# Kernel optimization log

Measured on AMD Instinct MI355X. Metric: run time of the kernel, lower is better.

Reference implementation:

```python
import jax, jax.numpy as jnp
import numpy as np

N_HEAD = 16

def setup_inputs() -> dict:
    key = jax.random.key(0)
    k1, k2 = jax.random.split(key)
    B, T, C = 4, 2048, 1024
    x = jax.random.normal(k1, (B, T, C), dtype=jnp.float32)
    # fused QKV projection weight, stored as [C, 3C] so qkv = x @ w_qkv
    # (equivalent to torch Linear(C, 3C, bias=False) with weight.T)
    w_qkv = jax.random.normal(k2, (C, 3 * C), dtype=jnp.float32) * (1.0 / np.sqrt(C))
    return {"x": x, "w_qkv": w_qkv}

def reference(x, w_qkv):
    B, T, C = x.shape
    H = N_HEAD
    D = C // H
    qkv = x @ w_qkv                                  # [B, T, 3C]
    q, k, v = jnp.split(qkv, 3, axis=2)              # each [B, T, C]
    q = q.reshape(B, T, H, D).transpose(0, 2, 1, 3)  # [B, H, T, D]
    k = k.reshape(B, T, H, D).transpose(0, 2, 1, 3)
    v = v.reshape(B, T, H, D).transpose(0, 2, 1, 3)
    scale = np.float32(1.0 / np.sqrt(D))
    att = jnp.einsum('bhqd,bhkd->bhqk', q, k) * scale   # [B, H, T, T]
    causal = jnp.tril(jnp.ones((T, T), dtype=bool))     # lower-tri = visible
    att = jnp.where(causal, att, -jnp.inf)
    att = jax.nn.softmax(att, axis=-1)
    out = jnp.einsum('bhqk,bhkd->bhqd', att, v)          # [B, H, T, D]
    return out.transpose(0, 2, 1, 3).reshape(B, T, C)
```

## Files before the change

### kernel.cpp

```cpp
#include <hip/hip_runtime.h>


#define B_ 4
#define T_ 2048
#define C_ 1024
#define H_ 16
#define D_ 64
#define QKV1 (B_*H_*T_*D_)

typedef __attribute__((ext_vector_type(4))) float  f32x4;
typedef __attribute__((ext_vector_type(8))) short  bf16x8;
typedef __attribute__((ext_vector_type(4))) short  bf16x4;

__device__ inline unsigned short f2bf(float f) {
  unsigned int u = __builtin_bit_cast(unsigned int, f);
  u += 0x7FFFu + ((u >> 16) & 1u);
  return (unsigned short)(u >> 16);
}

__device__ inline void gload16(const unsigned short* g, unsigned short* l) {
  __builtin_amdgcn_global_load_lds(
      (const __attribute__((address_space(1))) void*)g,
      (__attribute__((address_space(3))) void*)l, 16, 0, 0);
}

__global__ __launch_bounds__(256) void prep(const float* __restrict__ x,
                                            unsigned short* __restrict__ xb,
                                            const float* __restrict__ w,
                                            unsigned short* __restrict__ wt) {
  if (blockIdx.x < 2048) {
    size_t i = ((size_t)blockIdx.x * 256 + threadIdx.x) * 16;
    f32x4 a = *(const f32x4*)(x + i);
    f32x4 b = *(const f32x4*)(x + i + 4);
    f32x4 c = *(const f32x4*)(x + i + 8);
    f32x4 d = *(const f32x4*)(x + i + 12);
    bf16x8 o0, o1;
#pragma unroll
    for (int j = 0; j < 4; j++) {
      o0[j]     = (short)f2bf(a[j]);
      o0[j + 4] = (short)f2bf(b[j]);
      o1[j]     = (short)f2bf(c[j]);
      o1[j + 4] = (short)f2bf(d[j]);
    }
    *(bf16x8*)(xb + i) = o0;
    *(bf16x8*)(xb + i + 8) = o1;
  } else {
    __shared__ float tile[32][33];
    const int bid = blockIdx.x - 2048;
    const int tx = threadIdx.x & 31, ty = threadIdx.x >> 5;
    const int n0 = (bid % 96) * 32, k0 = (bid / 96) * 32;
#pragma unroll
    for (int j = 0; j < 4; j++) {
      int k = ty + j * 8;
      tile[k][tx] = w[(size_t)(k0 + k) * 3072 + n0 + tx];
    }
    __syncthreads();
#pragma unroll
    for (int j = 0; j < 4; j++) {
      int n = ty + j * 8;
      wt[(size_t)(n0 + n) * 1024 + k0 + tx] = f2bf(tile[tx][n]);
    }
  }
}

__global__ __launch_bounds__(256) void qkv_gemm(const unsigned short* __restrict__ xb,
                                                const unsigned short* __restrict__ wt,
                                                unsigned short* __restrict__ qkv) {
  __shared__ unsigned short Al[128 * 64];
  __shared__ unsigned short Bl[128 * 64];
  const int tid = threadIdx.x;
  const int lane = tid & 63, wid = tid >> 6;
  const int l15 = lane & 15, g = lane >> 4;
  const int m0 = blockIdx.y * 128, n0 = blockIdx.x * 128;
  const int wm = (wid >> 1) * 64, wn = (wid & 1) * 64;

  f32x4 acc[4][4] = {};

  const int srow[4] = { (0 * 256 + tid) >> 3, (1 * 256 + tid) >> 3,
                        (2 * 256 + tid) >> 3, (3 * 256 + tid) >> 3 };
  int scol[4];
#pragma unroll
  for (int sw = 0; sw < 4; sw++) {
    int s = sw * 256 + tid;
    scol[sw] = (s & 7) ^ (srow[sw] & 7);
  }

  for (int k0 = 0; k0 < 1024; k0 += 64) {
    __syncthreads();
#pragma unroll
    for (int sw = 0; sw < 4; sw++) {
      unsigned short* ldsA = &Al[(sw * 256 + wid * 64) * 8];
      unsigned short* ldsB = &Bl[(sw * 256 + wid * 64) * 8];
      gload16(xb + (size_t)(m0 + srow[sw]) * 1024 + k0 + scol[sw] * 8, ldsA);
      gload16(wt + (size_t)(n0 + srow[sw]) * 1024 + k0 + scol[sw] * 8, ldsB);
    }
    __syncthreads();

#pragma unroll
    for (int ks = 0; ks < 2; ks++) {
      bf16x8 af[4], bfr[4];
#pragma unroll
      for (int mt = 0; mt < 4; mt++) {
        int row = wm + mt * 16 + l15;
        int c = (ks * 4 + g) ^ (row & 7);
        af[mt] = *(const bf16x8*)&Al[(row * 8 + c) * 8];
      }
#pragma unroll
      for (int nt = 0; nt < 4; nt++) {
        int row = wn + nt * 16 + l15;
        int c = (ks * 4 + g) ^ (row & 7);
        bfr[nt] = *(const bf16x8*)&Bl[(row * 8 + c) * 8];
      }
#pragma unroll
      for (int mt = 0; mt < 4; mt++)
#pragma unroll
        for (int nt = 0; nt < 4; nt++)
          acc[mt][nt] = __builtin_amdgcn_mfma_f32_16x16x32_bf16(af[mt], bfr[nt], acc[mt][nt], 0, 0, 0);
    }
  }

  const int r0 = g * 4, cc = l15;
#pragma unroll
  for (int mt = 0; mt < 4; mt++)
#pragma unroll
    for (int nt = 0; nt < 4; nt++)
#pragma unroll
      for (int r = 0; r < 4; r++) {
        int m = m0 + wm + mt * 16 + r0 + r;
        int n = n0 + wn + nt * 16 + cc;
        int b = m >> 11, t = m & 2047;
        int which = n >> 10, c = n & 1023;
        int h = c >> 6, d = c & 63;
        qkv[(size_t)which * QKV1 + ((size_t)((b * H_ + h) * T_ + t)) * D_ + d] =
            f2bf(acc[mt][nt][r]);
      }
}

__global__ __launch_bounds__(256, 2) void attn(const unsigned short* __restrict__ qkv,
                                               float* __restrict__ out) {
  __shared__ unsigned short Kl[64][72];
  __shared__ unsigned short Vl[64][72];
  __shared__ unsigned short Pl[4][16][72];
  __shared__ float RSb[4][16], RSa[4][16];
  const int tid = threadIdx.x, lane = tid & 63, wq = tid >> 6;
  const int l15 = lane & 15, g = lane >> 4;
  const int bh = blockIdx.y;
  const int tt = bh >> 4;
  const int uu = ((int)blockIdx.x + (tt >> 1)) & 15;
  const int px = (tt & 1) ? (15 - uu) : uu;
  const int qta = px, qtb = 31 - px;
  const int ntiles = qtb + 1;
  const size_t base = (size_t)bh * (T_ * D_);
  const unsigned short* qp = qkv + base;
  const unsigned short* kp = qkv + (size_t)QKV1 + base;
  const unsigned short* vp = qkv + 2 * (size_t)QKV1 + base;

  bf16x8 qfa[2], qfb[2];
#define LOADQ(QF, Q0)                                                          \
  do {                                                                         \
    int qrow_ = (Q0) + wq * 16 + l15;                                          \
    _Pragma("unroll")                                                          \
    for (int kc = 0; kc < 2; kc++) {                                           \
      bf16x8 v = *(const bf16x8*)(qp + (size_t)qrow_ * 64 + kc * 32 + g * 8);  \
      _Pragma("unroll")                                                        \
      for (int j = 0; j < 8; j++) {                                            \
        unsigned short u = (unsigned short)v[j];                               \
        int e = u & 0x7F80;                                                    \
        u = (e > (3 << 7)) ? (unsigned short)(u - (3 << 7))                    \
                           : (unsigned short)(u & 0x8000);                     \
        v[j] = (short)u;                                                       \
      }                                                                        \
      QF[kc] = v;                                                              \
    }                                                                          \
  } while (0)
  LOADQ(qfa, qta * 64);
  LOADQ(qfb, qtb * 64);

  f32x4 oa[4] = {}, ob[4] = {};
  float rsa = 0.f, rsb = 0.f;

  bf16x8 kreg0, kreg1, vreg0, vreg1;
  const int krow = tid >> 3, kch = tid & 7;
  const int vpr = tid >> 3, vdch = tid & 7;
#define LOADKV(IT)                                                             \
  do {                                                                         \
    size_t k0_ = (size_t)(IT) * 64;                                            \
    kreg0 = *(const bf16x8*)(kp + (k0_ + krow) * 64 + kch * 8);                \
    kreg1 = *(const bf16x8*)(kp + (k0_ + 32 + krow) * 64 + kch * 8);           \
    vreg0 = *(const bf16x8*)(vp + (k0_ + 2 * vpr) * 64 + vdch * 8);            \
    vreg1 = *(const bf16x8*)(vp + (k0_ + 2 * vpr + 1) * 64 + vdch * 8);        \
  } while (0)

#define SOFTMAXT(S, RS, Q0, ISDIAG, K0)                                        \
  do {                                                                         \
    if (ISDIAG) {                                                              \
      _Pragma("unroll")                                                        \
      for (int nt = 0; nt < 4; nt++) {                                         \
        _Pragma("unroll")                                                      \
        for (int r = 0; r < 4; r++) {                                          \
          int kg_ = (K0) + nt * 16 + g * 4 + r;                                \
          if (kg_ > (Q0) + wq * 16 + l15) S[nt][r] = -1e30f;                   \
        }                                                                      \
      }                                                                        \
    }                                                                          \
    _Pragma("unroll")                                                          \
    for (int nt = 0; nt < 4; nt++) {                                           \
      bf16x4 pw_;                                                              \
      _Pragma("unroll")                                                        \
      for (int r = 0; r < 4; r++) {                                            \
        float p_ = __expf(S[nt][r]);                                           \
        RS += p_;                                                              \
        pw_[r] = (short)f2bf(p_);                                              \
      }                                                                        \
      *(bf16x4*)&Pl[wq][l15][nt * 16 + g * 4] = pw_;                           \
    }                                                                          \
  } while (0)

  LOADKV(0);
  for (int it = 0; it < ntiles; ++it) {
    __syncthreads();
    *(bf16x8*)&Kl[krow][kch * 8] = kreg0;
    *(bf16x8*)&Kl[32 + krow][kch * 8] = kreg1;
#pragma unroll
    for (int j = 0; j < 8; j++) {
      int d = vdch * 8 + j;
      unsigned int pk = ((unsigned int)(unsigned short)vreg1[j] << 16) |
                        (unsigned int)(unsigned short)vreg0[j];
      *(unsigned int*)&Vl[d][(2 * vpr) ^ ((d >> 3) << 3)] = pk;
    }
    if (it + 1 < ntiles) LOADKV(it + 1);
    __syncthreads();

    const bool doA = (it <= qta);

    f32x4 sb[4], sa[4];
    __builtin_amdgcn_s_setprio(1);
#pragma unroll
    for (int nt = 0; nt < 4; nt++) {
      bf16x8 kf0 = *(const bf16x8*)&Kl[nt * 16 + l15][g * 8];
      bf16x8 kf1 = *(const bf16x8*)&Kl[nt * 16 + l15][32 + g * 8];
      f32x4 t0 = {0.f, 0.f, 0.f, 0.f};
      t0 = __builtin_amdgcn_mfma_f32_16x16x32_bf16(kf0, qfb[0], t0, 0, 0, 0);
      t0 = __builtin_amdgcn_mfma_f32_16x16x32_bf16(kf1, qfb[1], t0, 0, 0, 0);
      sb[nt] = t0;
      if (doA) {
        f32x4 t1 = {0.f, 0.f, 0.f, 0.f};
        t1 = __builtin_amdgcn_mfma_f32_16x16x32_bf16(kf0, qfa[0], t1, 0, 0, 0);
        t1 = __builtin_amdgcn_mfma_f32_16x16x32_bf16(kf1, qfa[1], t1, 0, 0, 0);
        sa[nt] = t1;
      }
    }
    __builtin_amdgcn_s_setprio(0);

    SOFTMAXT(sb, rsb, qtb * 64, it == qtb, it * 64);
    asm volatile("s_waitcnt lgkmcnt(0)" ::: "memory");
    bf16x8 pb0 = *(const bf16x8*)&Pl[wq][l15][g * 8];
    bf16x8 pb1 = *(const bf16x8*)&Pl[wq][l15][32 + g * 8];

    bf16x8 pa0, pa1;
    if (doA) {
      SOFTMAXT(sa, rsa, qta * 64, it == qta, it * 64);
      asm volatile("s_waitcnt lgkmcnt(0)" ::: "memory");
      pa0 = *(const bf16x8*)&Pl[wq][l15][g * 8];
      pa1 = *(const bf16x8*)&Pl[wq][l15][32 + g * 8];
    }

    __builtin_amdgcn_s_setprio(1);
#pragma unroll
    for (int dt = 0; dt < 4; dt++) {
      int d_ = dt * 16 + l15;
      int sw_ = (d_ >> 3) << 3;
      bf16x8 vf0 = *(const bf16x8*)&Vl[d_][(g * 8) ^ sw_];
      bf16x8 vf1 = *(const bf16x8*)&Vl[d_][(32 + g * 8) ^ sw_];
      ob[dt] = __builtin_amdgcn_mfma_f32_16x16x32_bf16(pb0, vf0, ob[dt], 0, 0, 0);
      ob[dt] = __builtin_amdgcn_mfma_f32_16x16x32_bf16(pb1, vf1, ob[dt], 0, 0, 0);
      if (doA) {
        oa[dt] = __builtin_amdgcn_mfma_f32_16x16x32_bf16(pa0, vf0, oa[dt], 0, 0, 0);
        oa[dt] = __builtin_amdgcn_mfma_f32_16x16x32_bf16(pa1, vf1, oa[dt], 0, 0, 0);
      }
    }
    __builtin_amdgcn_s_setprio(0);
  }

  {
    float tb = rsb;
    tb += __shfl_xor(tb, 16); tb += __shfl_xor(tb, 32);
    float ta = rsa;
    ta += __shfl_xor(ta, 16); ta += __shfl_xor(ta, 32);
    if (g == 0) {
      RSb[wq][l15] = 1.0f / tb;
      RSa[wq][l15] = 1.0f / ta;
    }
  }
  asm volatile("s_waitcnt lgkmcnt(0)" ::: "memory");
  const int b = bh >> 4, h = bh & 15;
#define EPILOG(OACC, RSL, Q0)                                                  \
  do {                                                                         \
    _Pragma("unroll")                                                          \
    for (int r = 0; r < 4; r++) {                                              \
      float inv_ = RSL[wq][g * 4 + r];                                         \
      int qg_ = (Q0) + wq * 16 + g * 4 + r;                                    \
      _Pragma("unroll")                                                        \
      for (int dt = 0; dt < 4; dt++)                                           \
        out[((size_t)(b * T_ + qg_)) * C_ + h * 64 + dt * 16 + l15] =          \
            OACC[dt][r] * inv_;                                                \
    }                                                                          \
  } while (0)
  EPILOG(ob, RSb, qtb * 64);
  EPILOG(oa, RSa, qta * 64);
}

extern "C" void kernel_launch(void* const* d_in, const int* in_sizes, int n_in,
                              void* d_out, int out_size, void* d_ws, size_t ws_size,
                              hipStream_t stream) {
  const float* x = (const float*)d_in[0];
  const float* w = (const float*)d_in[1];
  float* out = (float*)d_out;
  unsigned short* wt  = (unsigned short*)d_ws;
  unsigned short* qkv = wt + (size_t)3072 * 1024;
  unsigned short* xb  = (unsigned short*)d_out;

  prep       <<<5120, 256, 0, stream>>>(x, xb, w, wt);
  qkv_gemm   <<<dim3(24, 64), 256, 0, stream>>>(xb, wt, qkv);
  attn       <<<dim3(16, 64), 256, 0, stream>>>(qkv, out);
}
```

Measured before the change: 145.2 us.

## Triple-buffer QKV GEMM with 256x128 tiles and 8 waves, interleaving prefetch with MFMA

Rewrites the QKV projection GEMM to use 512-thread blocks with 256x128 output tiles and a 3-stage LDS ring filled by async global-to-LDS loads. Each iteration issues the next-next tile's loads in slices between MFMA groups and uses a vmcnt wait plus a single barrier, instead of two barriers with no overlap. It also raises wave priority around the MFMAs. The aim is to hide global load latency and cut synchronisation in the GEMM. In exchange it uses more LDS (about 144KB) per block, which lowers occupancy, and adds hand-tuned waitcnt logic.

```diff
diff --git a/kernel.cpp b/kernel.cpp
--- a/kernel.cpp
+++ b/kernel.cpp
@@ -63,76 +63,112 @@
   }
 }
 
-__global__ __launch_bounds__(256) void qkv_gemm(const unsigned short* __restrict__ xb,
+__global__ __launch_bounds__(512) void qkv_gemm(const unsigned short* __restrict__ xb,
                                                 const unsigned short* __restrict__ wt,
                                                 unsigned short* __restrict__ qkv) {
-  __shared__ unsigned short Al[128 * 64];
-  __shared__ unsigned short Bl[128 * 64];
+  __shared__ unsigned short Al[3][256 * 64];
+  __shared__ unsigned short Bl[3][128 * 64];
   const int tid = threadIdx.x;
   const int lane = tid & 63, wid = tid >> 6;
   const int l15 = lane & 15, g = lane >> 4;
-  const int m0 = blockIdx.y * 128, n0 = blockIdx.x * 128;
-  const int wm = (wid >> 1) * 64, wn = (wid & 1) * 64;
-
-  f32x4 acc[4][4] = {};
-
-  const int srow[4] = { (0 * 256 + tid) >> 3, (1 * 256 + tid) >> 3,
-                        (2 * 256 + tid) >> 3, (3 * 256 + tid) >> 3 };
-  int scol[4];
+  const int m0 = blockIdx.y * 256, n0 = blockIdx.x * 128;
+  const int wr = wid >> 2, wc = wid & 3;
+
+  f32x4 acc[8][2] = {};
+
+  int arow[4], acol[4], brow[2], bcol[2];
 #pragma unroll
   for (int sw = 0; sw < 4; sw++) {
-    int s = sw * 256 + tid;
-    scol[sw] = (s & 7) ^ (srow[sw] & 7);
-  }
-
-  for (int k0 = 0; k0 < 1024; k0 += 64) {
-    __syncthreads();
-#pragma unroll
-    for (int sw = 0; sw < 4; sw++) {
-      unsigned short* ldsA = &Al[(sw * 256 + wid * 64) * 8];
-      unsigned short* ldsB = &Bl[(sw * 256 + wid * 64) * 8];
-      gload16(xb + (size_t)(m0 + srow[sw]) * 1024 + k0 + scol[sw] * 8, ldsA);
-      gload16(wt + (size_t)(n0 + srow[sw]) * 1024 + k0 + scol[sw] * 8, ldsB);
-    }
-    __syncthreads();
-
-#pragma unroll
-    for (int ks = 0; ks < 2; ks++) {
-      bf16x8 af[4], bfr[4];
-#pragma unroll
-      for (int mt = 0; mt < 4; mt++) {
-        int row = wm + mt * 16 + l15;
+    int s = sw * 512 + tid;
+    arow[sw] = s >> 3;
+    acol[sw] = (s & 7) ^ (arow[sw] & 7);
+  }
+#pragma unroll
+  for (int sw = 0; sw < 2; sw++) {
+    int s = sw * 512 + tid;
+    brow[sw] = s >> 3;
+    bcol[sw] = (s & 7) ^ (brow[sw] & 7);
+  }
+
+#define STAGE_A(BUF, T, SW)                                                    \
+  gload16(xb + (size_t)(m0 + arow[SW]) * 1024 + (T) * 64 + acol[SW] * 8,       \
+          &Al[BUF][((SW) * 512 + wid * 64) * 8])
+#define STAGE_B(BUF, T, SW)                                                    \
+  gload16(wt + (size_t)(n0 + brow[SW]) * 1024 + (T) * 64 + bcol[SW] * 8,       \
+          &Bl[BUF][((SW) * 512 + wid * 64) * 8])
+
+#pragma unroll
+  for (int sw = 0; sw < 4; sw++) STAGE_A(0, 0, sw);
+#pragma unroll
+  for (int sw = 0; sw < 2; sw++) STAGE_B(0, 0, sw);
+#pragma unroll
+  for (int sw = 0; sw < 4; sw++) STAGE_A(1, 1, sw);
+#pragma unroll
+  for (int sw = 0; sw < 2; sw++) STAGE_B(1, 1, sw);
+
+  for (int t = 0; t < 16; ++t) {
+    const int buf = t % 3;
+    const int nbuf = (t + 2) % 3;
+    const bool more = (t + 2) < 16;
+    if (t < 15) asm volatile("s_waitcnt vmcnt(6)" ::: "memory");
+    else        asm volatile("s_waitcnt vmcnt(0)" ::: "memory");
+    __builtin_amdgcn_s_barrier();
+    asm volatile("" ::: "memory");
+
+    bf16x8 bfr[2][2];
+#pragma unroll
+    for (int nt = 0; nt < 2; nt++)
+#pragma unroll
+      for (int ks = 0; ks < 2; ks++) {
+        int row = wc * 32 + nt * 16 + l15;
         int c = (ks * 4 + g) ^ (row & 7);
-        af[mt] = *(const bf16x8*)&Al[(row * 8 + c) * 8];
-      }
-#pragma unroll
-      for (int nt = 0; nt < 4; nt++) {
-        int row = wn + nt * 16 + l15;
-        int c = (ks * 4 + g) ^ (row & 7);
-        bfr[nt] = *(const bf16x8*)&Bl[(row * 8 + c) * 8];
-      }
-#pragma unroll
-      for (int mt = 0; mt < 4; mt++)
-#pragma unroll
-        for (int nt = 0; nt < 4; nt++)
-          acc[mt][nt] = __builtin_amdgcn_mfma_f32_16x16x32_bf16(af[mt], bfr[nt], acc[mt][nt], 0, 0, 0);
+        bfr[nt][ks] = *(const bf16x8*)&Bl[buf][(row * 8 + c) * 8];
+      }
+
+#pragma unroll
+    for (int q = 0; q < 4; q++) {
+      bf16x8 af[2][2];
+#pragma unroll
+      for (int m = 0; m < 2; m++)
+#pragma unroll
+        for (int ks = 0; ks < 2; ks++) {
+          int row = wr * 128 + (q * 2 + m) * 16 + l15;
+          int c = (ks * 4 + g) ^ (row & 7);
+          af[m][ks] = *(const bf16x8*)&Al[buf][(row * 8 + c) * 8];
+        }
+      if (more) {
+        if (q == 0)      { STAGE_A(nbuf, t + 2, 0); STAGE_A(nbuf, t + 2, 1); }
+        else if (q == 1) { STAGE_A(nbuf, t + 2, 2); STAGE_A(nbuf, t + 2, 3); }
+        else if (q == 2) { STAGE_B(nbuf, t + 2, 0); }
+        else             { STAGE_B(nbuf, t + 2, 1); }
+      }
+      __builtin_amdgcn_s_setprio(1);
+#pragma unroll
+      for (int m = 0; m < 2; m++)
+#pragma unroll
+        for (int nt = 0; nt < 2; nt++)
+#pragma unroll
+          for (int ks = 0; ks < 2; ks++)
+            acc[q * 2 + m][nt] = __builtin_amdgcn_mfma_f32_16x16x32_bf16(
+                af[m][ks], bfr[nt][ks], acc[q * 2 + m][nt], 0, 0, 0);
+      __builtin_amdgcn_s_setprio(0);
     }
   }
 
   const int r0 = g * 4, cc = l15;
 #pragma unroll
-  for (int mt = 0; mt < 4; mt++)
-#pragma unroll
-    for (int nt = 0; nt < 4; nt++)
+  for (int mr = 0; mr < 8; mr++)
+#pragma unroll
+    for (int nt = 0; nt < 2; nt++)
 #pragma unroll
       for (int r = 0; r < 4; r++) {
-        int m = m0 + wm + mt * 16 + r0 + r;
-        int n = n0 + wn + nt * 16 + cc;
-        int b = m >> 11, t = m & 2047;
+        int m = m0 + wr * 128 + mr * 16 + r0 + r;
+        int n = n0 + wc * 32 + nt * 16 + cc;
+        int b = m >> 11, tt = m & 2047;
         int which = n >> 10, c = n & 1023;
         int h = c >> 6, d = c & 63;
-        qkv[(size_t)which * QKV1 + ((size_t)((b * H_ + h) * T_ + t)) * D_ + d] =
-            f2bf(acc[mt][nt][r]);
+        qkv[(size_t)which * QKV1 + ((size_t)((b * H_ + h) * T_ + tt)) * D_ + d] =
+            f2bf(acc[mr][nt][r]);
       }
 }
 
@@ -321,6 +357,6 @@
   unsigned short* xb  = (unsigned short*)d_out;
 
   prep       <<<5120, 256, 0, stream>>>(x, xb, w, wt);
-  qkv_gemm   <<<dim3(24, 64), 256, 0, stream>>>(xb, wt, qkv);
+  qkv_gemm   <<<dim3(24, 32), 512, 0, stream>>>(xb, wt, qkv);
   attn       <<<dim3(16, 64), 256, 0, stream>>>(qkv, out);
 }
```

Result: slower. 153.7 us (+5.9%).
